# Kernel optimization log

Measured on AMD Instinct MI355X. Metric: run time of the kernel, lower is better.

## Reference

```python
import jax, jax.numpy as jnp
import numpy as np

MARGIN = 0.3
NEG_FILL = -100.0
EPS = 1e-6


def setup_inputs() -> dict:
    key = jax.random.key(0)
    k1, k2, k3 = jax.random.split(key, 3)
    B, N, D = 256, 131072, 128
    xembs = jax.random.normal(k1, (B, D), dtype=jnp.float32)
    yembs = jax.random.normal(k2, (N, D), dtype=jnp.float32)
    pos_inds = jax.random.randint(k3, (B, 1), 0, N, dtype=jnp.int64)
    # target: multi-hot label matrix; positives marked 1 at pos_inds
    target = jnp.zeros((B, N), dtype=jnp.float32)
    target = target.at[jnp.arange(B)[:, None], pos_inds].set(1.0)
    return {"xembs": xembs, "yembs": yembs, "target": target,
            "pos_inds": pos_inds, "num_neg": 5}


def reference(xembs, yembs, target, pos_inds, num_neg):
    # sim: [B, N]
    sim = xembs @ yembs.T
    # positive similarities: [B, 1]
    sim_p = jnp.take_along_axis(sim, pos_inds, axis=1)
    # mask out positives, mine hardest negatives
    neg_sim = jnp.where(target < EPS, sim, NEG_FILL)
    _, idx = jax.lax.top_k(neg_sim, num_neg)          # [B, num_neg]
    sim_n = jnp.take_along_axis(sim, idx, axis=1)      # [B, num_neg]
    # hinge triplet loss
    loss = jnp.maximum(jnp.zeros_like(sim_n), sim_n - sim_p + MARGIN)
    mask = (loss != 0).astype(loss.dtype)
    prob = jax.nn.softmax(sim_n * mask, axis=1)
    return (loss * prob).mean()
```

## Files before the change

### kernel.cpp

```cpp
#include <hip/hip_runtime.h>

#define BROWS 256
#define NCOLS 131072
#define DDIM  128
#define K     5
#define MARGIN 0.3f

#define NBLK  512
#define CPB   (NCOLS / NBLK)
#define NIT   (CPB / 16)
#define ZGATE 3.4f
#define RCAP  96
#define YSTR  68

typedef __attribute__((ext_vector_type(8))) __bf16 bf16x8;
typedef __attribute__((ext_vector_type(4))) float f32x4;
typedef __attribute__((ext_vector_type(4))) unsigned int u32x4;

__device__ __forceinline__ unsigned pack_bf16(float a, float b) {
#if defined(__has_builtin) && __has_builtin(__builtin_amdgcn_cvt_pk_bf16_f32)
    auto r = __builtin_amdgcn_cvt_pk_bf16_f32(a, b);
    return __builtin_bit_cast(unsigned, r);
#else
    unsigned ua = __float_as_uint(a), ub = __float_as_uint(b);
    unsigned ra = (ua + 0x7fffu + ((ua >> 16) & 1u)) >> 16;
    unsigned rb = (ub + 0x7fffu + ((ub >> 16) & 1u)) & 0xffff0000u;
    return ra | rb;
#endif
}

__device__ __forceinline__ u32x4 pack8(const float4& a, const float4& b) {
    u32x4 t;
    t[0] = pack_bf16(a.x, a.y); t[1] = pack_bf16(a.z, a.w);
    t[2] = pack_bf16(b.x, b.y); t[3] = pack_bf16(b.z, b.w);
    return t;
}

__global__ __launch_bounds__(256, 2) void gemm_collect_kernel(
    const float* __restrict__ x, const float* __restrict__ y,
    uint2* __restrict__ regions, int* __restrict__ nbs, float* __restrict__ outz)
{
    __shared__ unsigned ybf[2][16 * YSTR];
    __shared__ int lcnt;

    const int tid   = threadIdx.x;
    const int lane  = tid & 63;
    const int quad  = lane >> 4;
    const int l15   = lane & 15;
    const int wrow0 = tid & 192;
    const int col0  = blockIdx.x * CPB;

    if (blockIdx.x == 0 && tid == 0) outz[0] = 0.f;
    if (tid == 0) lcnt = 0;

    bf16x8 af[4][4];
    float nrm[4];
#pragma unroll
    for (int mt = 0; mt < 4; ++mt) {
        const float* xp = x + (size_t)(wrow0 + mt * 16 + l15) * DDIM + quad * 8;
        float s2 = 0.f;
#pragma unroll
        for (int s = 0; s < 4; ++s) {
            const float4 a = *(const float4*)(xp + s * 32);
            const float4 b = *(const float4*)(xp + s * 32 + 4);
            s2 = fmaf(a.x, a.x, s2); s2 = fmaf(a.y, a.y, s2);
            s2 = fmaf(a.z, a.z, s2); s2 = fmaf(a.w, a.w, s2);
            s2 = fmaf(b.x, b.x, s2); s2 = fmaf(b.y, b.y, s2);
            s2 = fmaf(b.z, b.z, s2); s2 = fmaf(b.w, b.w, s2);
            const u32x4 t = pack8(a, b);
            af[mt][s] = __builtin_bit_cast(bf16x8, t);
        }
        nrm[mt] = s2;
    }
    float myThr[4];
#pragma unroll
    for (int mt = 0; mt < 4; ++mt) {
        float s2 = nrm[mt];
        s2 += __shfl_xor(s2, 16);
        s2 += __shfl_xor(s2, 32);
        myThr[mt] = ZGATE * sqrtf(s2);
    }
    float thrv[16];
#pragma unroll
    for (int mt = 0; mt < 4; ++mt)
#pragma unroll
        for (int r = 0; r < 4; ++r)
            thrv[mt * 4 + r] = __shfl(myThr[mt], quad * 4 + r);

    const int sc = tid >> 4, sj = tid & 15;
    const float* ysrc = y + (size_t)(col0 + sc) * DDIM + sj * 8;
    const unsigned sdst = sc * YSTR + sj * 4;
    const unsigned frag_off = l15 * YSTR + quad * 4;

    float4 ga[2], gb[2];
    ga[0] = *(const float4*)(ysrc);
    gb[0] = *(const float4*)(ysrc + 4);
    ga[1] = *(const float4*)(ysrc + 16 * DDIM);
    gb[1] = *(const float4*)(ysrc + 16 * DDIM + 4);
    *(u32x4*)(&ybf[0][0] + sdst) = pack8(ga[0], gb[0]);

    for (int it = 0; it < NIT; ++it) {
        if (it + 2 < NIT) {
            const float* yn = ysrc + (size_t)(it + 2) * 16 * DDIM;
            ga[it & 1] = *(const float4*)(yn);
            gb[it & 1] = *(const float4*)(yn + 4);
        }
        __syncthreads();

        const unsigned* yb = &ybf[it & 1][0];
        bf16x8 bfrag[4];
#pragma unroll
        for (int s = 0; s < 4; ++s)
            bfrag[s] = __builtin_bit_cast(bf16x8, *(const u32x4*)(yb + frag_off + s * 16));

        f32x4 acc[4];
#pragma unroll
        for (int mt = 0; mt < 4; ++mt) acc[mt] = (f32x4){0.f, 0.f, 0.f, 0.f};
#pragma unroll
        for (int s = 0; s < 4; ++s)
#pragma unroll
            for (int mt = 0; mt < 4; ++mt)
                acc[mt] = __builtin_amdgcn_mfma_f32_16x16x32_bf16(af[mt][s], bfrag[s], acc[mt], 0, 0, 0);

        if (it + 1 < NIT)
            *(u32x4*)(&ybf[(it + 1) & 1][0] + sdst) = pack8(ga[(it + 1) & 1], gb[(it + 1) & 1]);

        float m = -1.f;
#pragma unroll
        for (int mt = 0; mt < 4; ++mt)
#pragma unroll
            for (int r = 0; r < 4; ++r)
                m = fmaxf(m, acc[mt][r] - thrv[mt * 4 + r]);
        if (m > 0.f) {
            const int col = col0 + it * 16 + l15;
#pragma unroll
            for (int mt = 0; mt < 4; ++mt)
#pragma unroll
                for (int r = 0; r < 4; ++r) {
                    const float v = acc[mt][r];
                    if (v > thrv[mt * 4 + r]) {
                        const int idx = atomicAdd(&lcnt, 1);
                        if (idx < RCAP) {
                            const int row = wrow0 + mt * 16 + quad * 4 + r;
                            regions[blockIdx.x * RCAP + idx] =
                                make_uint2(__float_as_uint(v), ((unsigned)row << 17) | (unsigned)col);
                        }
                    }
                }
        }
    }

    __syncthreads();
    if (tid == 0) nbs[blockIdx.x] = lcnt;
}

__device__ __forceinline__ void insert5(float* t5, float v) {
    if (v > t5[K - 1]) {
        float nv = v;
#pragma unroll
        for (int p = 0; p < K; ++p) {
            const bool gt = nv > t5[p];
            const float tv = t5[p];
            if (gt) { t5[p] = nv; nv = tv; }
        }
    }
}

__device__ __forceinline__ void merge5(float* __restrict__ t5, const float* __restrict__ src) {
#pragma unroll
    for (int p = 0; p < K; ++p) insert5(t5, src[p]);
}

__device__ __forceinline__ float epilogue(const float* t5, float sp) {
    float loss[K], logit[K];
#pragma unroll
    for (int p = 0; p < K; ++p) {
        loss[p]  = fmaxf(0.f, t5[p] - sp + MARGIN);
        logit[p] = (loss[p] != 0.f) ? t5[p] : 0.f;
    }
    float mx = logit[0];
#pragma unroll
    for (int p = 1; p < K; ++p) mx = fmaxf(mx, logit[p]);
    float den = 0.f, num = 0.f;
#pragma unroll
    for (int p = 0; p < K; ++p) {
        const float e = __expf(logit[p] - mx);
        den += e;
        num += loss[p] * e;
    }
    return num / den;
}

__global__ __launch_bounds__(256) void reduce_kernel(
    const float* __restrict__ x, const float* __restrict__ y,
    const int* __restrict__ pos,
    const uint2* __restrict__ regions, const int* __restrict__ nbs,
    int* __restrict__ flag, float* __restrict__ out)
{
    const int row = blockIdx.x;
    const int tid = threadIdx.x;
    __shared__ float sred[256];
    __shared__ float sv[256 * K];
    __shared__ int sover;
    if (tid == 0) sover = 0;

    const int prow = pos[row];
    float p = 0.f;
    if (tid < DDIM) p = x[row * DDIM + tid] * y[(size_t)prow * DDIM + tid];
    sred[tid] = p;
    __syncthreads();
    for (int s = 128; s >= 1; s >>= 1) {
        if (tid < s) sred[tid] += sred[tid + s];
        __syncthreads();
    }

    float t5[K];
#pragma unroll
    for (int q = 0; q < K; ++q) t5[q] = -3.0e38f;
    int over = 0;
    for (int reg = tid; reg < NBLK; reg += 256) {
        int nb = nbs[reg];
        if (nb > RCAP) { over = 1; nb = RCAP; }
        const uint2* rp = regions + (size_t)reg * RCAP;
        for (int i = 0; i < nb; ++i) {
            const uint2 e = rp[i];
            const int r = (int)(e.y >> 17), c = (int)(e.y & 0x1FFFFu);
            if (r == row && c != prow) insert5(t5, __uint_as_float(e.x));
        }
    }
    if (over) sover = 1;

#pragma unroll
    for (int q = 0; q < K; ++q) sv[tid * K + q] = t5[q];
    __syncthreads();
    for (int s = 128; s >= 1; s >>= 1) {
        if (tid < s) {
            merge5(t5, &sv[(tid + s) * K]);
#pragma unroll
            for (int q = 0; q < K; ++q) sv[tid * K + q] = t5[q];
        }
        __syncthreads();
    }

    if (tid == 0) {
        const bool ok = (sover == 0) && (t5[K - 1] > -1.0e38f);
        flag[row] = ok ? 0 : 1;
        if (ok) atomicAdd(out, epilogue(t5, sred[0]) * (1.0f / (BROWS * K)));
    }
}

__global__ __launch_bounds__(256) void fallback_kernel(
    const float* __restrict__ x, const float* __restrict__ y,
    const int* __restrict__ pos, const int* __restrict__ flag,
    float* __restrict__ out)
{
    const int row = blockIdx.x;
    if (flag[row] == 0) return;
    const int tid = threadIdx.x;
    const int prow = pos[row];
    __shared__ float xr[DDIM];
    __shared__ float sv[256 * K];
    if (tid < DDIM) xr[tid] = x[row * DDIM + tid];
    __syncthreads();

    float t5[K];
#pragma unroll
    for (int q = 0; q < K; ++q) t5[q] = -3.0e38f;
    for (int col = tid; col < NCOLS; col += 256) {
        if (col == prow) continue;
        const float* yp = y + (size_t)col * DDIM;
        float d = 0.f;
        for (int k = 0; k < DDIM; ++k) d = fmaf(xr[k], yp[k], d);
        insert5(t5, d);
    }
#pragma unroll
    for (int q = 0; q < K; ++q) sv[tid * K + q] = t5[q];
    __syncthreads();
    for (int s = 128; s >= 1; s >>= 1) {
        if (tid < s) {
            merge5(t5, &sv[(tid + s) * K]);
#pragma unroll
            for (int q = 0; q < K; ++q) sv[tid * K + q] = t5[q];
        }
        __syncthreads();
    }
    if (tid == 0) {
        float sp = 0.f;
        const float* yp = y + (size_t)prow * DDIM;
        for (int k = 0; k < DDIM; ++k) sp = fmaf(xr[k], yp[k], sp);
        atomicAdd(out, epilogue(t5, sp) * (1.0f / (BROWS * K)));
    }
}

extern "C" void kernel_launch(void* const* d_in, const int* in_sizes, int n_in,
                              void* d_out, int out_size, void* d_ws, size_t ws_size,
                              hipStream_t stream) {
    const float* x  = (const float*)d_in[0];
    const float* y  = (const float*)d_in[1];
    const int* pos  = (const int*)d_in[3];

    uint2* regions = (uint2*)d_ws;
    int*   nbs     = (int*)(regions + (size_t)NBLK * RCAP);
    int*   flag    = nbs + NBLK;

    gemm_collect_kernel<<<dim3(NBLK), 256, 0, stream>>>(x, y, regions, nbs, (float*)d_out);
    reduce_kernel<<<dim3(BROWS), 256, 0, stream>>>(x, y, pos, regions, nbs, flag, (float*)d_out);
    fallback_kernel<<<dim3(BROWS), 256, 0, stream>>>(x, y, pos, flag, (float*)d_out);
}
```

Before: 269.9 us.

## Preload all Y tile slices into registers and fold fallback into reduce kernel

```diff
diff --git a/kernel.cpp b/kernel.cpp
--- a/kernel.cpp
+++ b/kernel.cpp
@@ -89,22 +89,20 @@
 
     const int sc = tid >> 4, sj = tid & 15;
     const float* ysrc = y + (size_t)(col0 + sc) * DDIM + sj * 8;
+    u32x4 yw[NIT];
+#pragma unroll
+    for (int t = 0; t < NIT; ++t) {
+        const float4 a = *(const float4*)(ysrc + (size_t)t * 16 * DDIM);
+        const float4 b = *(const float4*)(ysrc + (size_t)t * 16 * DDIM + 4);
+        yw[t] = pack8(a, b);
+    }
+
     const unsigned sdst = sc * YSTR + sj * 4;
     const unsigned frag_off = l15 * YSTR + quad * 4;
-
-    float4 ga[2], gb[2];
-    ga[0] = *(const float4*)(ysrc);
-    gb[0] = *(const float4*)(ysrc + 4);
-    ga[1] = *(const float4*)(ysrc + 16 * DDIM);
-    gb[1] = *(const float4*)(ysrc + 16 * DDIM + 4);
-    *(u32x4*)(&ybf[0][0] + sdst) = pack8(ga[0], gb[0]);
-
+    *(u32x4*)(&ybf[0][0] + sdst) = yw[0];
+
+#pragma unroll
     for (int it = 0; it < NIT; ++it) {
-        if (it + 2 < NIT) {
-            const float* yn = ysrc + (size_t)(it + 2) * 16 * DDIM;
-            ga[it & 1] = *(const float4*)(yn);
-            gb[it & 1] = *(const float4*)(yn + 4);
-        }
         __syncthreads();
 
         const unsigned* yb = &ybf[it & 1][0];
@@ -123,7 +121,7 @@
                 acc[mt] = __builtin_amdgcn_mfma_f32_16x16x32_bf16(af[mt][s], bfrag[s], acc[mt], 0, 0, 0);
 
         if (it + 1 < NIT)
-            *(u32x4*)(&ybf[(it + 1) & 1][0] + sdst) = pack8(ga[(it + 1) & 1], gb[(it + 1) & 1]);
+            *(u32x4*)(&ybf[(it + 1) & 1][0] + sdst) = yw[it + 1];
 
         float m = -1.f;
 #pragma unroll
@@ -195,18 +193,23 @@
     const float* __restrict__ x, const float* __restrict__ y,
     const int* __restrict__ pos,
     const uint2* __restrict__ regions, const int* __restrict__ nbs,
-    int* __restrict__ flag, float* __restrict__ out)
+    float* __restrict__ out)
 {
     const int row = blockIdx.x;
     const int tid = threadIdx.x;
     __shared__ float sred[256];
     __shared__ float sv[256 * K];
-    __shared__ int sover;
-    if (tid == 0) sover = 0;
+    __shared__ float xr[DDIM];
+    __shared__ int sover, sok;
+    if (tid == 0) { sover = 0; sok = 0; }
 
     const int prow = pos[row];
     float p = 0.f;
-    if (tid < DDIM) p = x[row * DDIM + tid] * y[(size_t)prow * DDIM + tid];
+    if (tid < DDIM) {
+        const float xv = x[row * DDIM + tid];
+        xr[tid] = xv;
+        p = xv * y[(size_t)prow * DDIM + tid];
+    }
     sred[tid] = p;
     __syncthreads();
     for (int s = 128; s >= 1; s >>= 1) {
@@ -244,52 +247,34 @@
 
     if (tid == 0) {
         const bool ok = (sover == 0) && (t5[K - 1] > -1.0e38f);
-        flag[row] = ok ? 0 : 1;
+        sok = ok ? 1 : 0;
         if (ok) atomicAdd(out, epilogue(t5, sred[0]) * (1.0f / (BROWS * K)));
     }
-}
-
-__global__ __launch_bounds__(256) void fallback_kernel(
-    const float* __restrict__ x, const float* __restrict__ y,
-    const int* __restrict__ pos, const int* __restrict__ flag,
-    float* __restrict__ out)
-{
-    const int row = blockIdx.x;
-    if (flag[row] == 0) return;
-    const int tid = threadIdx.x;
-    const int prow = pos[row];
-    __shared__ float xr[DDIM];
-    __shared__ float sv[256 * K];
-    if (tid < DDIM) xr[tid] = x[row * DDIM + tid];
-    __syncthreads();
-
-    float t5[K];
-#pragma unroll
-    for (int q = 0; q < K; ++q) t5[q] = -3.0e38f;
+    __syncthreads();
+    if (sok) return;
+
+    float b5[K];
+#pragma unroll
+    for (int q = 0; q < K; ++q) b5[q] = -3.0e38f;
     for (int col = tid; col < NCOLS; col += 256) {
         if (col == prow) continue;
         const float* yp = y + (size_t)col * DDIM;
         float d = 0.f;
         for (int k = 0; k < DDIM; ++k) d = fmaf(xr[k], yp[k], d);
-        insert5(t5, d);
-    }
-#pragma unroll
-    for (int q = 0; q < K; ++q) sv[tid * K + q] = t5[q];
+        insert5(b5, d);
+    }
+#pragma unroll
+    for (int q = 0; q < K; ++q) sv[tid * K + q] = b5[q];
     __syncthreads();
     for (int s = 128; s >= 1; s >>= 1) {
         if (tid < s) {
-            merge5(t5, &sv[(tid + s) * K]);
-#pragma unroll
-            for (int q = 0; q < K; ++q) sv[tid * K + q] = t5[q];
-        }
-        __syncthreads();
-    }
-    if (tid == 0) {
-        float sp = 0.f;
-        const float* yp = y + (size_t)prow * DDIM;
-        for (int k = 0; k < DDIM; ++k) sp = fmaf(xr[k], yp[k], sp);
-        atomicAdd(out, epilogue(t5, sp) * (1.0f / (BROWS * K)));
-    }
+            merge5(b5, &sv[(tid + s) * K]);
+#pragma unroll
+            for (int q = 0; q < K; ++q) sv[tid * K + q] = b5[q];
+        }
+        __syncthreads();
+    }
+    if (tid == 0) atomicAdd(out, epilogue(b5, sred[0]) * (1.0f / (BROWS * K)));
 }
 
 extern "C" void kernel_launch(void* const* d_in, const int* in_sizes, int n_in,
@@ -301,9 +286,7 @@
 
     uint2* regions = (uint2*)d_ws;
     int*   nbs     = (int*)(regions + (size_t)NBLK * RCAP);
-    int*   flag    = nbs + NBLK;
 
     gemm_collect_kernel<<<dim3(NBLK), 256, 0, stream>>>(x, y, regions, nbs, (float*)d_out);
-    reduce_kernel<<<dim3(BROWS), 256, 0, stream>>>(x, y, pos, regions, nbs, flag, (float*)d_out);
-    fallback_kernel<<<dim3(BROWS), 256, 0, stream>>>(x, y, pos, flag, (float*)d_out);
-}
+    reduce_kernel<<<dim3(BROWS), 256, 0, stream>>>(x, y, pos, regions, nbs, (float*)d_out);
+}
```

After: 246.5 us. -8.7%, faster.
